# Optimization experiments

Measured on AMD Instinct MI355X. Metric: run time of the kernel, lower is better.

The kernel has to match this reference:

```python
import jax, jax.numpy as jnp
import numpy as np

B, L, E, H = 4, 2048, 512, 8


def setup_inputs() -> dict:
    key = jax.random.key(0)
    ks = jax.random.split(key, 12)
    s = 0.02
    inp = {
        "values": jax.random.normal(ks[0], (B, L, E), jnp.float32),
        "keys": jax.random.normal(ks[1], (B, L, E), jnp.float32),
        "queries": jax.random.normal(ks[2], (B, L, E), jnp.float32),
    }
    mask = jax.random.randint(ks[3], (B, L, H, H), 0, 2, jnp.int32)
    # guarantee at least one unmasked entry per softmax row to avoid NaN rows
    mask = mask.at[..., 0].set(1)
    inp["mask"] = mask
    # Linear(E, E*H) weights stored as (in, out); torch uses y = x @ W.T + b
    inp["Wv"] = jax.random.normal(ks[4], (E, E * H), jnp.float32) * s
    inp["bv"] = jnp.zeros((E * H,), jnp.float32)
    inp["Wk"] = jax.random.normal(ks[5], (E, E * H), jnp.float32) * s
    inp["bk"] = jnp.zeros((E * H,), jnp.float32)
    inp["Wq"] = jax.random.normal(ks[6], (E, E * H), jnp.float32) * s
    inp["bq"] = jnp.zeros((E * H,), jnp.float32)
    inp["Wo"] = jax.random.normal(ks[7], (E * H, E), jnp.float32) * s
    inp["bo"] = jnp.zeros((E,), jnp.float32)
    return inp


def reference(values, keys, queries, mask, Wv, bv, Wk, bk, Wq, bq, Wo, bo):
    b, l, e = queries.shape
    h = Wq.shape[1] // e

    def proj(x, W, bias):
        # (B,L,E) -> (B,L,H,E) -> transpose(1,2) -> (B,H,L,E)
        return (x @ W + bias).reshape(b, -1, h, e).transpose(0, 2, 1, 3)

    v = proj(values, Wv, bv)
    k = proj(keys, Wk, bk)
    q = proj(queries, Wq, bq)
    # Faithful to source: einsum labels applied to the TRANSPOSED (B,H,L,E)
    # tensors, so 'q'/'k' bind to the heads axis and 'h' binds to seq axis.
    # energy: (B, L, H, H) -- head-vs-head scores at each position.
    energy = jnp.einsum('nqhd,nkhd->nhqk', q, k)
    energy = jnp.where(mask == 0, -jnp.inf, energy)
    attn = jax.nn.softmax(energy / jnp.sqrt(jnp.float32(e)), axis=3)
    # out of einsum: (B, H, L, E); raw row-major reshape to (B, L, H*E)
    out = jnp.einsum('nhql,nlhd->nqhd', attn, v).reshape(b, -1, h * e)
    return out @ Wo + bo
```

## Files before the change

### kernel.cpp

```cpp
#include <hip/hip_runtime.h>
#include <stdint.h>

typedef __attribute__((ext_vector_type(4))) float f32x4;
typedef __attribute__((ext_vector_type(8))) __bf16 bf16x8;

__device__ __forceinline__ unsigned short f2bf(float f) {
  union { float f; uint32_t u; } v; v.f = f;
  uint32_t u = v.u;
  return (unsigned short)((u + 0x7FFFu + ((u >> 16) & 1u)) >> 16);
}
__device__ __forceinline__ float bflo(uint32_t u) {
  union { uint32_t u; float f; } v; v.u = u << 16; return v.f;
}
__device__ __forceinline__ float bfhi(uint32_t u) {
  union { uint32_t u; float f; } v; v.u = u & 0xffff0000u; return v.f;
}

__device__ __forceinline__ void async_copy16(void* lds, const void* g) {
  __builtin_amdgcn_global_load_lds(
      (const __attribute__((address_space(1))) void*)g,
      (__attribute__((address_space(3))) void*)lds,
      16, 0, 0);
}

__global__ void cvt3_f32_bf16(const float* __restrict__ in0,
                              const float* __restrict__ in1,
                              const float* __restrict__ in2,
                              uint32_t* __restrict__ out, int n) {
  const float* in = (blockIdx.y == 0) ? in0 : (blockIdx.y == 1) ? in1 : in2;
  uint32_t* o = out + (size_t)blockIdx.y * (n / 2);
  int i = blockIdx.x * blockDim.x + threadIdx.x;
  int idx = i * 8;
  if (idx >= n) return;
  float4 a = *(const float4*)(in + idx);
  float4 b = *(const float4*)(in + idx + 4);
  uint4 ov;
  ov.x = f2bf(a.x) | ((uint32_t)f2bf(a.y) << 16);
  ov.y = f2bf(a.z) | ((uint32_t)f2bf(a.w) << 16);
  ov.z = f2bf(b.x) | ((uint32_t)f2bf(b.y) << 16);
  ov.w = f2bf(b.z) | ((uint32_t)f2bf(b.w) << 16);
  *(uint4*)(o + i * 4) = ov;
}

__global__ void transpose3_to_bf16(const float* __restrict__ in0,
                                   const float* __restrict__ in1,
                                   const float* __restrict__ in2,
                                   unsigned short* __restrict__ out,
                                   int R, int C) {
  const float* in = (blockIdx.z == 0) ? in0 : (blockIdx.z == 1) ? in1 : in2;
  unsigned short* o = out + (size_t)blockIdx.z * ((size_t)R * C);
  __shared__ float tile[32][33];
  int c0 = blockIdx.x * 32, r0 = blockIdx.y * 32;
  int tx = threadIdx.x, ty = threadIdx.y;
  #pragma unroll
  for (int rr = 0; rr < 32; rr += 8)
    tile[ty + rr][tx] = in[(size_t)(r0 + ty + rr) * C + c0 + tx];
  __syncthreads();
  #pragma unroll
  for (int rr = 0; rr < 32; rr += 8)
    o[(size_t)(c0 + ty + rr) * R + r0 + tx] = f2bf(tile[tx][ty + rr]);
}

__global__ void transpose_to_bf16(const float* __restrict__ in,
                                  unsigned short* __restrict__ out,
                                  int R, int C) {
  __shared__ float tile[32][33];
  int c0 = blockIdx.x * 32, r0 = blockIdx.y * 32;
  int tx = threadIdx.x, ty = threadIdx.y;
  #pragma unroll
  for (int rr = 0; rr < 32; rr += 8)
    tile[ty + rr][tx] = in[(size_t)(r0 + ty + rr) * C + c0 + tx];
  __syncthreads();
  #pragma unroll
  for (int rr = 0; rr < 32; rr += 8)
    out[(size_t)(c0 + ty + rr) * R + r0 + tx] = f2bf(tile[tx][ty + rr]);
}

template <int NK, int NN, bool PARTIAL, bool DUAL>
__global__ __launch_bounds__(512, 2) void gemm256(
    const unsigned short* __restrict__ A,
    const unsigned short* __restrict__ Bt,
    const float* __restrict__ bias,
    void* __restrict__ Cout,
    const unsigned short* __restrict__ A2,
    const unsigned short* __restrict__ Bt2,
    const float* __restrict__ bias2,
    void* __restrict__ Cout2,
    int Mt, int NtG, int KC, int Kfull) {
  constexpr int TT = NK * NN;
  static_assert(TT >= 4 && (TT % 2) == 0, "need even TT >= 4");
  __shared__ unsigned short lds[2 * 2 * 256 * 64];

  const int nwg = Mt * NtG * KC;
  const int cpx = nwg >> 3;
  const int bid = blockIdx.x;
  const int nb = (bid & 7) * cpx + (bid >> 3);
  const int kc = nb / (Mt * NtG);
  const int r2 = nb % (Mt * NtG);
  const int bm = r2 / NtG;
  const int ng = r2 % NtG;
  const int mat = DUAL ? (ng >> 3) : 0;
  const int ngm = DUAL ? (ng & 7) : ng;
  const int N = (DUAL ? (NtG >> 1) : NtG) * NN * 256;
  const size_t koff = (size_t)kc * (NK * 64);

  const unsigned short* Asrc = (DUAL && mat) ? A2 : A;
  const unsigned short* Bsrc = (DUAL && mat) ? Bt2 : Bt;
  const float* biasd = (DUAL && mat) ? bias2 : bias;
  void* Cd = (DUAL && mat) ? Cout2 : Cout;

  const int tid = threadIdx.x;
  const int wv = tid >> 6, ln = tid & 63;
  const int wm = wv >> 2, wn = wv & 3;

  f32x4 acc[8][4] = {};
  bf16x8 af[4][2];
  bf16x8 bfb[2][2];

  char* const lds0 = (char*)lds;
  char* const lds1 = (char*)lds + 65536;

  auto stage_tile = [&](int tt, char* dst) {
    const int kt = tt % NK;
    const int bnn = ngm * NN + tt / NK;
    #pragma unroll
    for (int i = 0; i < 4; ++i) {
      const int rb = i * 64 + wv * 8;
      const int row = rb + (ln >> 3);
      const int kcs = (ln & 7) ^ (row & 7);
      async_copy16(dst + rb * 128,
                   Asrc + (size_t)(bm * 256 + row) * Kfull + koff + kt * 64 + kcs * 8);
      async_copy16(dst + 32768 + rb * 128,
                   Bsrc + (size_t)(bnn * 256 + row) * Kfull + koff + kt * 64 + kcs * 8);
    }
  };
  auto load_af = [&](int mh, const char* buf) {
    #pragma unroll
    for (int f = 0; f < 4; ++f) {
      const int lr = wm * 128 + (mh * 4 + f) * 16 + (ln & 15);
      #pragma unroll
      for (int s = 0; s < 2; ++s) {
        const int kq = s * 4 + (ln >> 4);
        af[f][s] = *(const bf16x8*)(buf + lr * 128 + ((kq ^ (lr & 7)) * 16));
      }
    }
  };
  auto load_bf = [&](int nh, const char* buf) {
    #pragma unroll
    for (int gq = 0; gq < 2; ++gq) {
      const int lr = wn * 64 + (nh * 2 + gq) * 16 + (ln & 15);
      #pragma unroll
      for (int s = 0; s < 2; ++s) {
        const int kq = s * 4 + (ln >> 4);
        bfb[gq][s] =
            *(const bf16x8*)(buf + 32768 + lr * 128 + ((kq ^ (lr & 7)) * 16));
      }
    }
  };
  auto mfma_quad = [&](int mh, int nh) {
    __builtin_amdgcn_s_setprio(1);
    #pragma unroll
    for (int s = 0; s < 2; ++s)
      #pragma unroll
      for (int f = 0; f < 4; ++f)
        #pragma unroll
        for (int gq = 0; gq < 2; ++gq)
          acc[mh * 4 + f][nh * 2 + gq] = __builtin_amdgcn_mfma_f32_16x16x32_bf16(
              bfb[gq][s], af[f][s], acc[mh * 4 + f][nh * 2 + gq], 0, 0, 0);
    __builtin_amdgcn_s_setprio(0);
  };
  auto epilogue = [&](int nt) {
    const int m0 = bm * 256 + wm * 128 + (ln & 15);
    const int n0 = (ngm * NN + nt) * 256 + wn * 64 + ((ln >> 4) << 2);
    if (PARTIAL) {
      float* Cp = (float*)Cd + (size_t)kc * ((size_t)Mt * 256) * N;
      #pragma unroll
      for (int f = 0; f < 8; ++f) {
        const int row = m0 + f * 16;
        #pragma unroll
        for (int g = 0; g < 4; ++g)
          *(f32x4*)(Cp + (size_t)row * N + n0 + g * 16) = acc[f][g];
      }
    } else {
      unsigned short* C = (unsigned short*)Cd;
      #pragma unroll
      for (int f = 0; f < 8; ++f) {
        const int row = m0 + f * 16;
        #pragma unroll
        for (int g = 0; g < 4; ++g) {
          const int col = n0 + g * 16;
          float4 bv = *(const float4*)(biasd + col);
          uint2 o;
          o.x = f2bf(acc[f][g][0] + bv.x) | ((uint32_t)f2bf(acc[f][g][1] + bv.y) << 16);
          o.y = f2bf(acc[f][g][2] + bv.z) | ((uint32_t)f2bf(acc[f][g][3] + bv.w) << 16);
          *(uint2*)(C + (size_t)row * N + col) = o;
        }
      }
    }
    #pragma unroll
    for (int f = 0; f < 8; ++f)
      #pragma unroll
      for (int g = 0; g < 4; ++g)
        acc[f][g] = (f32x4){0.f, 0.f, 0.f, 0.f};
  };

  auto tile_body = [&](int tau, const char* buf, char* obuf) {
    if (tau + 1 < TT) stage_tile(tau + 1, obuf);
    load_af(0, buf); load_bf(0, buf);
    mfma_quad(0, 0);
    __builtin_amdgcn_sched_barrier(0);
    load_bf(1, buf);
    mfma_quad(0, 1);
    __builtin_amdgcn_sched_barrier(0);
    load_af(1, buf);
    mfma_quad(1, 1);
    __builtin_amdgcn_sched_barrier(0);
    load_bf(0, buf);
    mfma_quad(1, 0);
    __builtin_amdgcn_sched_barrier(0);
    if (tau + 1 < TT)
      asm volatile("s_waitcnt vmcnt(0)" ::: "memory");
    __builtin_amdgcn_s_barrier();
    if ((tau + 1) % NK == 0) epilogue(tau / NK);
  };

  stage_tile(0, lds0);
  asm volatile("s_waitcnt vmcnt(0)" ::: "memory");
  __builtin_amdgcn_sched_barrier(0);
  __builtin_amdgcn_s_barrier();

  for (int it = 0; it < TT / 2; ++it) {
    tile_body(2 * it,     lds0, lds1);
    tile_body(2 * it + 1, lds1, lds0);
  }
}

__global__ void reduce4_bias(const float* __restrict__ p,
                             const float* __restrict__ bo,
                             float* __restrict__ out) {
  const size_t S = (size_t)8192 * 512;
  size_t i = ((size_t)blockIdx.x * 256 + threadIdx.x) * 4;
  float4 a = *(const float4*)(p + i);
  float4 b = *(const float4*)(p + S + i);
  float4 c = *(const float4*)(p + 2 * S + i);
  float4 d = *(const float4*)(p + 3 * S + i);
  float4 bb = *(const float4*)(bo + (int)(i & 511));
  float4 o;
  o.x = a.x + b.x + c.x + d.x + bb.x;
  o.y = a.y + b.y + c.y + d.y + bb.y;
  o.z = a.z + b.z + c.z + d.z + bb.z;
  o.w = a.w + b.w + c.w + d.w + bb.w;
  *(float4*)(out + i) = o;
}

__global__ __launch_bounds__(256) void energy_mfma(
    const unsigned short* __restrict__ Q,
    const unsigned short* __restrict__ Kb,
    const int* __restrict__ mask,
    float* __restrict__ P) {
  const int wave = threadIdx.x >> 6, ln = threadIdx.x & 63;
  const int t2 = (blockIdx.x * 4 + wave) * 2;
  const int r16 = ln & 15;
  const int g = ln >> 4;
  const size_t rowoff = (size_t)(t2 + (r16 >> 3)) * 4096 + (r16 & 7) * 512 + g * 8;
  const unsigned short* qb = Q + rowoff;
  const unsigned short* kb = Kb + rowoff;

  f32x4 acc = {};
  #pragma unroll
  for (int s = 0; s < 16; ++s) {
    bf16x8 qf = *(const bf16x8*)(qb + s * 32);
    bf16x8 kf = *(const bf16x8*)(kb + s * 32);
    acc = __builtin_amdgcn_mfma_f32_16x16x32_bf16(qf, kf, acc, 0, 0, 0);
  }

  const int ct = r16 >> 3, j = r16 & 7;
  const bool valid = ((g >> 1) == ct);
  const int tok = t2 + ct;
  float pv[4];
  #pragma unroll
  for (int r = 0; r < 4; ++r) {
    const int i = (g & 1) * 4 + r;
    float e = acc[r] * 0.044194173824159216f;
    int mk = 1;
    if (valid) mk = mask[(size_t)tok * 64 + i * 8 + j];
    if (mk == 0) e = -1e30f;
    float m = e;
    m = fmaxf(m, __shfl_xor(m, 1, 64));
    m = fmaxf(m, __shfl_xor(m, 2, 64));
    m = fmaxf(m, __shfl_xor(m, 4, 64));
    float p = __expf(e - m);
    float sum = p;
    sum += __shfl_xor(sum, 1, 64);
    sum += __shfl_xor(sum, 2, 64);
    sum += __shfl_xor(sum, 4, 64);
    pv[r] = p / sum;
  }
  if (valid) {
    #pragma unroll
    for (int r = 0; r < 4; ++r) {
      const int i = (g & 1) * 4 + r;
      P[(size_t)tok * 64 + i * 8 + j] = pv[r];
    }
  }
}

__global__ __launch_bounds__(256) void pv_kernel(
    const float* __restrict__ P,
    const unsigned short* __restrict__ Vb,
    unsigned short* __restrict__ out2) {
  const int wave = threadIdx.x >> 6, lane = threadIdx.x & 63;
  const int t = blockIdx.x * 4 + wave;
  const unsigned short* Vr = Vb + (size_t)t * 4096;
  float att = P[(size_t)t * 64 + lane];

  uint4 v4[8];
  #pragma unroll
  for (int jj = 0; jj < 8; ++jj)
    v4[jj] = *(const uint4*)(Vr + jj * 512 + lane * 8);

  const int nb = t >> 11, l = t & 2047;
  const size_t tok_base = (size_t)nb * 8388608 + (size_t)(l >> 3) * 4096 +
                          (size_t)(l & 7) * 512 + lane * 8;
  #pragma unroll
  for (int hh = 0; hh < 8; ++hh) {
    float accv[8] = {0.f, 0.f, 0.f, 0.f, 0.f, 0.f, 0.f, 0.f};
    #pragma unroll
    for (int jj = 0; jj < 8; ++jj) {
      float a = __shfl(att, hh * 8 + jj, 64);
      accv[0] += a * bflo(v4[jj].x); accv[1] += a * bfhi(v4[jj].x);
      accv[2] += a * bflo(v4[jj].y); accv[3] += a * bfhi(v4[jj].y);
      accv[4] += a * bflo(v4[jj].z); accv[5] += a * bfhi(v4[jj].z);
      accv[6] += a * bflo(v4[jj].w); accv[7] += a * bfhi(v4[jj].w);
    }
    uint4 o;
    o.x = f2bf(accv[0]) | ((uint32_t)f2bf(accv[1]) << 16);
    o.y = f2bf(accv[2]) | ((uint32_t)f2bf(accv[3]) << 16);
    o.z = f2bf(accv[4]) | ((uint32_t)f2bf(accv[5]) << 16);
    o.w = f2bf(accv[6]) | ((uint32_t)f2bf(accv[7]) << 16);
    *(uint4*)(out2 + tok_base + (size_t)hh * 1048576) = o;
  }
}

extern "C" void kernel_launch(void* const* d_in, const int* in_sizes, int n_in,
                              void* d_out, int out_size, void* d_ws, size_t ws_size,
                              hipStream_t stream) {
  const float* values  = (const float*)d_in[0];
  const float* keys    = (const float*)d_in[1];
  const float* queries = (const float*)d_in[2];
  const int*   mask    = (const int*)d_in[3];
  const float* Wv = (const float*)d_in[4];
  const float* bv = (const float*)d_in[5];
  const float* Wk = (const float*)d_in[6];
  const float* bk = (const float*)d_in[7];
  const float* Wq = (const float*)d_in[8];
  const float* bq = (const float*)d_in[9];
  const float* Wo = (const float*)d_in[10];
  const float* bo = (const float*)d_in[11];

  unsigned short* xv  = (unsigned short*)d_ws;
  unsigned short* xk  = xv + 8192 * 512;
  unsigned short* xq  = xk + 8192 * 512;
  unsigned short* Wvt = xq + 8192 * 512;
  unsigned short* Wkt = Wvt + 4096 * 512;
  unsigned short* Wqt = Wkt + 4096 * 512;
  unsigned short* Wot = Wqt + 4096 * 512;
  float*          P   = (float*)(Wot + 4096 * 512);
  unsigned short* bufA = (unsigned short*)(P + 8192 * 64);
  unsigned short* bufB = bufA + (size_t)8192 * 4096;

  const int nx = 8192 * 512;
  cvt3_f32_bf16<<<dim3(nx / 8 / 256, 3), 256, 0, stream>>>(
      values, keys, queries, (uint32_t*)xv, nx);

  transpose3_to_bf16<<<dim3(4096 / 32, 512 / 32, 3), dim3(32, 8), 0, stream>>>(
      Wv, Wk, Wq, Wvt, 512, 4096);
  transpose_to_bf16<<<dim3(512 / 32, 4096 / 32), dim3(32, 8), 0, stream>>>(
      Wo, Wot, 4096, 512);

  gemm256<8, 2, false, true><<<512, 512, 0, stream>>>(
      xq, Wqt, bq, bufA, xk, Wkt, bk, bufB, 32, 16, 1, 512);

  energy_mfma<<<8192 / 8, 256, 0, stream>>>(bufA, bufB, mask, P);

  gemm256<8, 2, false, false><<<256, 512, 0, stream>>>(
      xv, Wvt, bv, bufA, nullptr, nullptr, nullptr, nullptr, 32, 8, 1, 512);

  pv_kernel<<<8192 / 4, 256, 0, stream>>>(P, bufA, bufB);

  gemm256<16, 1, true, false><<<256, 512, 0, stream>>>(
      bufB, Wot, nullptr, (float*)bufA, nullptr, nullptr, nullptr, nullptr,
      32, 2, 4, 4096);
  reduce4_bias<<<4096, 256, 0, stream>>>((float*)bufA, bo, (float*)d_out);
}
```

Before: 265.1 us.

## Add triple-buffered GEMM with K-step 32 for V and output projections

Adds a new GEMM kernel, gemm_tb, that uses three LDS buffers with K-tiles of 32 instead of two buffers. Loads are prefetched two tiles ahead and the barrier waits only on older loads (vmcnt(4)), so memory latency overlaps more with MFMA work. The V projection and the split-K output projection switch to it, with tile counts doubled to keep the same K coverage. The cost is more barriers per unit of K and smaller per-tile MFMA batches, which could offset the deeper prefetch.

```diff
diff --git a/kernel.cpp b/kernel.cpp
--- a/kernel.cpp
+++ b/kernel.cpp
@@ -235,6 +235,130 @@
   }
 }
 
+template <int NK, int NN, bool PARTIAL>
+__global__ __launch_bounds__(512, 1) void gemm_tb(
+    const unsigned short* __restrict__ A,
+    const unsigned short* __restrict__ Bt,
+    const float* __restrict__ bias,
+    void* __restrict__ Cout,
+    int Mt, int NtG, int KC, int Kfull) {
+  constexpr int TT = NK * NN;
+  static_assert(TT >= 4, "need >=4 tiles");
+  __shared__ unsigned short lds[3 * 2 * 256 * 32];
+
+  const int nwg = Mt * NtG * KC;
+  const int cpx = nwg >> 3;
+  const int bid = blockIdx.x;
+  const int nb = (bid & 7) * cpx + (bid >> 3);
+  const int kc = nb / (Mt * NtG);
+  const int r2 = nb % (Mt * NtG);
+  const int bm = r2 / NtG;
+  const int ng = r2 % NtG;
+  const int N = NtG * NN * 256;
+  const size_t koff = (size_t)kc * (NK * 32);
+
+  const int tid = threadIdx.x;
+  const int wv = tid >> 6, ln = tid & 63;
+  const int wm = wv >> 2, wn = wv & 3;
+
+  f32x4 acc[8][4] = {};
+  bf16x8 af[8];
+  bf16x8 bfb[4];
+
+  auto stage_tile = [&](int tt, char* dst) {
+    const int kt = tt % NK;
+    const int bnn = ng * NN + tt / NK;
+    #pragma unroll
+    for (int j = 0; j < 2; ++j) {
+      const int lr = j * 128 + wv * 16 + (ln >> 2);
+      const int srcslot = (ln & 3) ^ ((lr >> 1) & 3);
+      async_copy16(dst + (j * 128 + wv * 16) * 64 + ln * 16,
+                   A + (size_t)(bm * 256 + lr) * Kfull + koff + kt * 32 + srcslot * 8);
+      async_copy16(dst + 16384 + (j * 128 + wv * 16) * 64 + ln * 16,
+                   Bt + (size_t)(bnn * 256 + lr) * Kfull + koff + kt * 32 + srcslot * 8);
+    }
+  };
+  auto load_frags = [&](const char* buf) {
+    const int kq = ln >> 4;
+    #pragma unroll
+    for (int f = 0; f < 8; ++f) {
+      const int lr = wm * 128 + f * 16 + (ln & 15);
+      af[f] = *(const bf16x8*)(buf + lr * 64 + ((kq ^ ((lr >> 1) & 3)) * 16));
+    }
+    #pragma unroll
+    for (int g = 0; g < 4; ++g) {
+      const int lr = wn * 64 + g * 16 + (ln & 15);
+      bfb[g] = *(const bf16x8*)(buf + 16384 + lr * 64 + ((kq ^ ((lr >> 1) & 3)) * 16));
+    }
+  };
+  auto epilogue = [&](int nt) {
+    const int m0 = bm * 256 + wm * 128 + (ln & 15);
+    const int n0 = (ng * NN + nt) * 256 + wn * 64 + ((ln >> 4) << 2);
+    if (PARTIAL) {
+      float* Cp = (float*)Cout + (size_t)kc * ((size_t)Mt * 256) * N;
+      #pragma unroll
+      for (int f = 0; f < 8; ++f) {
+        const int row = m0 + f * 16;
+        #pragma unroll
+        for (int g = 0; g < 4; ++g)
+          *(f32x4*)(Cp + (size_t)row * N + n0 + g * 16) = acc[f][g];
+      }
+    } else {
+      unsigned short* C = (unsigned short*)Cout;
+      #pragma unroll
+      for (int f = 0; f < 8; ++f) {
+        const int row = m0 + f * 16;
+        #pragma unroll
+        for (int g = 0; g < 4; ++g) {
+          const int col = n0 + g * 16;
+          float4 bv = *(const float4*)(bias + col);
+          uint2 o;
+          o.x = f2bf(acc[f][g][0] + bv.x) | ((uint32_t)f2bf(acc[f][g][1] + bv.y) << 16);
+          o.y = f2bf(acc[f][g][2] + bv.z) | ((uint32_t)f2bf(acc[f][g][3] + bv.w) << 16);
+          *(uint2*)(C + (size_t)row * N + col) = o;
+        }
+      }
+    }
+    #pragma unroll
+    for (int f = 0; f < 8; ++f)
+      #pragma unroll
+      for (int g = 0; g < 4; ++g)
+        acc[f][g] = (f32x4){0.f, 0.f, 0.f, 0.f};
+  };
+
+  char* b0 = (char*)lds;
+  char* b1 = (char*)lds + 32768;
+  char* b2 = (char*)lds + 65536;
+
+  stage_tile(0, b0);
+  stage_tile(1, b1);
+  asm volatile("s_waitcnt vmcnt(4)" ::: "memory");
+  __builtin_amdgcn_sched_barrier(0);
+  __builtin_amdgcn_s_barrier();
+
+  for (int t = 0; t < TT; ++t) {
+    if (t + 2 < TT) stage_tile(t + 2, b2);
+    load_frags(b0);
+    __builtin_amdgcn_s_setprio(1);
+    #pragma unroll
+    for (int f = 0; f < 8; ++f)
+      #pragma unroll
+      for (int g = 0; g < 4; ++g)
+        acc[f][g] = __builtin_amdgcn_mfma_f32_16x16x32_bf16(
+            bfb[g], af[f], acc[f][g], 0, 0, 0);
+    __builtin_amdgcn_s_setprio(0);
+    __builtin_amdgcn_sched_barrier(0);
+    if (t + 2 < TT) {
+      asm volatile("s_waitcnt vmcnt(4)" ::: "memory");
+    } else if (t + 1 < TT) {
+      asm volatile("s_waitcnt vmcnt(0)" ::: "memory");
+    }
+    __builtin_amdgcn_s_barrier();
+    if ((t + 1) % NK == 0) epilogue(t / NK);
+    char* tmp = b0; b0 = b1; b1 = b2; b2 = tmp;
+  }
+}
+
 __global__ void reduce4_bias(const float* __restrict__ p,
                              const float* __restrict__ bo,
                              float* __restrict__ out) {
@@ -383,13 +507,12 @@
 
   energy_mfma<<<8192 / 8, 256, 0, stream>>>(bufA, bufB, mask, P);
 
-  gemm256<8, 2, false, false><<<256, 512, 0, stream>>>(
-      xv, Wvt, bv, bufA, nullptr, nullptr, nullptr, nullptr, 32, 8, 1, 512);
+  gemm_tb<16, 2, false><<<256, 512, 0, stream>>>(
+      xv, Wvt, bv, bufA, 32, 8, 1, 512);
 
   pv_kernel<<<8192 / 4, 256, 0, stream>>>(P, bufA, bufB);
 
-  gemm256<16, 1, true, false><<<256, 512, 0, stream>>>(
-      bufB, Wot, nullptr, (float*)bufA, nullptr, nullptr, nullptr, nullptr,
-      32, 2, 4, 4096);
+  gemm_tb<32, 1, true><<<256, 512, 0, stream>>>(
+      bufB, Wot, nullptr, (float*)bufA, 32, 2, 4, 4096);
   reduce4_bias<<<4096, 256, 0, stream>>>((float*)bufA, bo, (float*)d_out);
 }
```

After: 262.6 us (median of 2 runs). Within noise of the previous version (-0.9%).
